# Kernel tuning notes

Hardware: AMD Instinct MI355X
Metric: run time of the kernel (lower is better)

Reference implementation:

```python
import jax, jax.numpy as jnp
import numpy as np

# TT embedding config
IN_SHAPE = (100, 100, 100)      # vocab = 1_000_000
OUT_SHAPE = (4, 8, 4)           # embed_dim = 128
RANKS = (1, 32, 32, 32, 16, 8, 1)
OUT_SIZE = int(np.prod(OUT_SHAPE))
VOCAB = int(np.prod(IN_SHAPE))

def _xavier(key, shape):
    fan_in, fan_out = shape[0] * shape[1], shape[1] * shape[2]
    a = float(np.sqrt(6.0 / (shape[0] * shape[1] * shape[2] / shape[1] + 0)))  # placeholder
    # torch xavier_uniform on (r0, n, r1): fan_in = n*r1? torch treats dim0 as fan_out-ish;
    # exact init scale does not affect correctness checking, use a simple uniform bound.
    bound = float(np.sqrt(6.0 / (shape[0] * shape[1] + shape[1] * shape[2])))
    return jax.random.uniform(key, shape, jnp.float32, -bound, bound)

def setup_inputs() -> dict:
    key = jax.random.key(0)
    ks = jax.random.split(key, 7)
    idx = jax.random.randint(ks[0], (512, 128), 0, VOCAB, dtype=jnp.int32)
    shapes = [(RANKS[i], s, RANKS[i + 1]) for i, s in enumerate(IN_SHAPE + OUT_SHAPE)]
    cores = [_xavier(ks[i + 1], shapes[i]) for i in range(6)]
    return {"idx": idx, "core0": cores[0], "core1": cores[1], "core2": cores[2],
            "core3": cores[3], "core4": cores[4], "core5": cores[5]}

def reference(idx, core0, core1, core2, core3, core4, core5):
    in_shape = idx.shape
    flat = idx.reshape(-1)  # [N]
    # index decomposition with tt_index_factor = [10000, 100]
    i0 = flat // 10000
    i1 = (flat % 10000) // 100
    i2 = flat % 100
    # per-index gather + chained small batched matmuls over input cores
    g = core0[0, i0, :]                              # [N, r1]
    g = jnp.einsum('nr,rns->ns', g, core1[:, i1, :])  # [N, r2]
    g = jnp.einsum('nr,rns->ns', g, core2[:, i2, :])  # [N, r3]
    # contract output cores into a single [r3, OUT_SIZE] matrix (shared across batch)
    t = core3.reshape(-1, core4.shape[0]) @ core4.reshape(core4.shape[0], -1)
    t = t.reshape(-1, core5.shape[0]) @ core5.reshape(core5.shape[0], -1)
    W = t.reshape(RANKS[3], OUT_SIZE)                # [r3, 128]
    out = g @ W                                      # [N, 128]
    return out.reshape(in_shape + (OUT_SIZE,))
```

## Files before the change

kernel.cpp:

```cpp
#include <hip/hip_runtime.h>

#define N_TOKENS   65536
#define TOKS_PER_BLK 128
#define MAIN_TILES (N_TOKENS / TOKS_PER_BLK + 100)
#define ORD_SIZE    (MAIN_TILES * TOKS_PER_BLK)
#define NB_M2   400
#define NB_G1T  1250
#define NB_HIST 64
#define PREP_BLOCKS (NB_M2 + NB_G1T + NB_HIST)

#define WS_M2T  0
#define WS_G1T  204800
#define WS_CNT  364800
#define WS_ORD  372992
#define WS_NEED ((size_t)(372992 + ORD_SIZE) * 4)

typedef __attribute__((ext_vector_type(8))) short bf16x8;
typedef __attribute__((ext_vector_type(4))) float f32x4;

__device__ __forceinline__ unsigned short f2bf(float x) {
    union { float f; unsigned u; } v; v.f = x;
    unsigned r = v.u + 0x7FFF + ((v.u >> 16) & 1);
    return (unsigned short)(r >> 16);
}

__global__ __launch_bounds__(256) void prep(
    const int* __restrict__ idx,
    const float* __restrict__ c0, const float* __restrict__ c1,
    const float* __restrict__ c2, const float* __restrict__ c3,
    const float* __restrict__ c4, const float* __restrict__ c5,
    unsigned short* __restrict__ M2T, unsigned short* __restrict__ G1Tb,
    int* __restrict__ cntT) {
    __shared__ float smem[5200];
    const int b = blockIdx.x, t = threadIdx.x;

    if (b < NB_M2) {
        const int i2 = b >> 2;
        const int p  = b & 3;
        float* c4l = smem;
        float* c5l = smem + 1024;
        float* t45 = smem + 1056;
        float* c3p = smem + 1568;
        float* Wl  = smem + 2080;
        float* c2l = smem + 3104;
        *(float4*)(c4l + t * 4) = *(const float4*)(c4 + t * 4);
        if (t < 8) *(float4*)(c5l + t * 4) = *(const float4*)(c5 + t * 4);
        if (t < 128) {
            const int r = t >> 2, q4 = (t & 3) * 4;
            *(float4*)(c3p + r * 16 + q4) = *(const float4*)(c3 + (r * 4 + p) * 16 + q4);
        }
        {
            const int r = t >> 3, s4 = (t & 7) * 4;
            const float4 v = *(const float4*)(c2 + r * 3200 + i2 * 32 + s4);
            c2l[r * 33 + s4 + 0] = v.x;
            c2l[r * 33 + s4 + 1] = v.y;
            c2l[r * 33 + s4 + 2] = v.z;
            c2l[r * 33 + s4 + 3] = v.w;
        }
        __syncthreads();
#pragma unroll
        for (int k = 0; k < 2; ++k) {
            const int e = t + k * 256;
            const int q = e >> 5, u = e & 31;
            const int m1 = u >> 2, v = u & 3;
            float acc = 0.f;
#pragma unroll
            for (int m2 = 0; m2 < 8; ++m2)
                acc = fmaf(c4l[q * 64 + m1 * 8 + m2], c5l[m2 * 4 + v], acc);
            t45[e] = acc;
        }
        __syncthreads();
#pragma unroll
        for (int k = 0; k < 4; ++k) {
            const int e = t + k * 256;
            const int s = e >> 5, jl = e & 31;
            float acc = 0.f;
#pragma unroll
            for (int q = 0; q < 16; ++q)
                acc = fmaf(c3p[s * 16 + q], t45[q * 32 + jl], acc);
            Wl[e] = acc;
        }
        __syncthreads();
#pragma unroll
        for (int k = 0; k < 4; ++k) {
            const int e = t + k * 256;
            const int jl = e >> 5, r = e & 31;
            float acc = 0.f;
#pragma unroll
            for (int s = 0; s < 32; ++s)
                acc = fmaf(c2l[r * 33 + s], Wl[s * 32 + jl], acc);
            M2T[i2 * 4096 + p * 1024 + e] = f2bf(acc);
        }
    } else if (b < NB_M2 + NB_G1T) {
        const int pair = (b - NB_M2) * 8 + (t >> 5);
        const int s = t & 31;
        const int i0 = pair / 100;
        const int i1 = pair - i0 * 100;
        const float4* a4 = (const float4*)(c0 + i0 * 32);
        const float* c1p = c1 + i1 * 32 + s;
        float acc = 0.f;
#pragma unroll
        for (int r4 = 0; r4 < 8; ++r4) {
            const float4 a = a4[r4];
            acc = fmaf(a.x, c1p[(r4 * 4 + 0) * 3200], acc);
            acc = fmaf(a.y, c1p[(r4 * 4 + 1) * 3200], acc);
            acc = fmaf(a.z, c1p[(r4 * 4 + 2) * 3200], acc);
            acc = fmaf(a.w, c1p[(r4 * 4 + 3) * 3200], acc);
        }
        G1Tb[pair * 32 + s] = f2bf(acc);
    } else {
        const int hb = b - (NB_M2 + NB_G1T);
        int* lh = (int*)smem;
        if (t < 128) lh[t] = 0;
        __syncthreads();
#pragma unroll
        for (int k = 0; k < 4; ++k) {
            const int n = hb * 1024 + k * 256 + t;
            atomicAdd(&lh[idx[n] % 100], 1);
        }
        __syncthreads();
        if (t < 128) cntT[t * 64 + hb] = lh[t];
    }
}

__global__ __launch_bounds__(256) void sort2(const int* __restrict__ idx,
                                             const int* __restrict__ cntT,
                                             int* __restrict__ order) {
    __shared__ int totals[100];
    __shared__ int offsj[100];
    __shared__ int sb[101];
    __shared__ int lhj[100];
    const int j = blockIdx.x, t = threadIdx.x;
    if (t < 100) {
        lhj[t] = 0;
        const int4* row = (const int4*)(cntT + t * 64);
        int tot = 0, off = 0;
#pragma unroll
        for (int i = 0; i < 16; ++i) {
            const int4 v = row[i];
            const int cb = i * 4;
            tot += v.x + v.y + v.z + v.w;
            if (cb + 0 < j) off += v.x;
            if (cb + 1 < j) off += v.y;
            if (cb + 2 < j) off += v.z;
            if (cb + 3 < j) off += v.w;
        }
        totals[t] = tot;
        offsj[t] = off;
    }
    __syncthreads();
    if (t < 64) {
        const int e0 = 2 * t, e1 = 2 * t + 1;
        const int p0 = (e0 < 100) ? ((totals[e0] + 127) & ~127) : 0;
        const int p1 = (e1 < 100) ? ((totals[e1] + 127) & ~127) : 0;
        const int pair = p0 + p1;
        int incl = pair;
#pragma unroll
        for (int d = 1; d < 64; d <<= 1) {
            const int v = __shfl_up(incl, d, 64);
            if (t >= d) incl += v;
        }
        const int base = incl - pair;
        if (e0 < 100) sb[e0] = base;
        if (e1 < 100) sb[e1] = base + p0;
        if (t == 63) sb[100] = incl;
    }
    __syncthreads();
    int bkt[4], rnk[4];
#pragma unroll
    for (int k = 0; k < 4; ++k) {
        const int n = j * 1024 + k * 256 + t;
        const int bb = idx[n] % 100;
        bkt[k] = bb;
        rnk[k] = atomicAdd(&lhj[bb], 1);
    }
#pragma unroll
    for (int k = 0; k < 4; ++k) {
        const int n = j * 1024 + k * 256 + t;
        order[sb[bkt[k]] + offsj[bkt[k]] + rnk[k]] = n;
    }
    for (int bb = j; bb < 100; bb += 64) {
        const int tot = totals[bb];
        const int pt = (tot + 127) & ~127;
        for (int i = tot + t; i < pt; i += 256) order[sb[bb] + i] = -1;
    }
    {
        const int gt = sb[100];
        for (int i = gt + j * 256 + t; i < ORD_SIZE; i += 64 * 256) order[i] = -1;
    }
}

__global__ __launch_bounds__(256) void tt_main(
    const int* __restrict__ idx, const int* __restrict__ order,
    const unsigned short* __restrict__ G1Tb, const unsigned short* __restrict__ M2T,
    float* __restrict__ out) {
    __shared__ unsigned short g1b[128 * 40];
    __shared__ unsigned short m2t[128 * 40];
    __shared__ int toks[TOKS_PER_BLK];

    const int t = threadIdx.x;
    const int base = blockIdx.x * TOKS_PER_BLK;
    const int n0 = order[base];
    if (n0 < 0) return;
    const int i2v = idx[n0] % 100;

    {
        const int tk = t >> 1, half = t & 1;
        const int n = order[base + tk];
        int4 v0 = {0, 0, 0, 0}, v1 = {0, 0, 0, 0};
        if (n >= 0) {
            const int pair = idx[n] / 100;
            const int4* g = (const int4*)(G1Tb + pair * 32);
            v0 = g[half * 2];
            v1 = g[half * 2 + 1];
        }
        int4* d = (int4*)(g1b + tk * 40 + half * 16);
        d[0] = v0;
        d[1] = v1;
        if (t < TOKS_PER_BLK) toks[t] = order[base + t];
    }
    {
        const int j = t >> 1, half = t & 1;
        const int4* s = (const int4*)(M2T + i2v * 4096 + j * 32);
        int4* d = (int4*)(m2t + j * 40 + half * 16);
        d[0] = s[half * 2];
        d[1] = s[half * 2 + 1];
    }
    __syncthreads();

    const int wid  = t >> 6;
    const int lane = t & 63;
    const int ln15 = lane & 15;
    const int q8   = (lane >> 4) * 8;

    f32x4 acc[2][8];
#pragma unroll
    for (int a = 0; a < 2; ++a)
#pragma unroll
        for (int c = 0; c < 8; ++c) acc[a][c] = (f32x4){0.f, 0.f, 0.f, 0.f};

    bf16x8 af[2], bfr[8];
#pragma unroll
    for (int trr = 0; trr < 2; ++trr) {
        const int tok = (2 * wid + trr) * 16 + ln15;
        af[trr] = *(const bf16x8*)(g1b + tok * 40 + q8);
    }
#pragma unroll
    for (int tc = 0; tc < 8; ++tc) {
        const int j = tc * 16 + ln15;
        bfr[tc] = *(const bf16x8*)(m2t + j * 40 + q8);
    }
#pragma unroll
    for (int trr = 0; trr < 2; ++trr)
#pragma unroll
        for (int tc = 0; tc < 8; ++tc)
            acc[trr][tc] = __builtin_amdgcn_mfma_f32_16x16x32_bf16(
                af[trr], bfr[tc], acc[trr][tc], 0, 0, 0);

    const int rowq = (lane >> 4) * 4;
#pragma unroll
    for (int trr = 0; trr < 2; ++trr) {
#pragma unroll
        for (int reg = 0; reg < 4; ++reg) {
            const int tokr = (2 * wid + trr) * 16 + rowq + reg;
            const int n = toks[tokr];
            if (n >= 0) {
                float* o = out + (size_t)n * 128 + ln15;
#pragma unroll
                for (int tc = 0; tc < 8; ++tc) o[tc * 16] = acc[trr][tc][reg];
            }
        }
    }
}

__global__ void build_w(const float* __restrict__ c3, const float* __restrict__ c4,
                        const float* __restrict__ c5, float* __restrict__ W) {
    int t = blockIdx.x * blockDim.x + threadIdx.x;
    if (t >= 32 * 128) return;
    int r = t >> 7;
    int j = t & 127;
    int p  = j >> 5;
    int m1 = (j >> 2) & 7;
    int v  = j & 3;
    const float* c3row = c3 + (r * 4 + p) * 16;
    float acc = 0.f;
#pragma unroll
    for (int m2 = 0; m2 < 8; ++m2) {
        float t1 = 0.f;
#pragma unroll
        for (int q = 0; q < 16; ++q)
            t1 += c3row[q] * c4[q * 64 + m1 * 8 + m2];
        acc += t1 * c5[m2 * 4 + v];
    }
    W[r * 128 + j] = acc;
}

__global__ __launch_bounds__(256, 4) void tt_embed_fb(
    const int* __restrict__ idx, const float* __restrict__ c0,
    const float* __restrict__ c1, const float* __restrict__ c2,
    const float* __restrict__ Wg, float* __restrict__ out) {
    __shared__ float Wl[32 * 128];
    __shared__ float g2l[8][32];
    const int t = threadIdx.x;
    {
        const float4* Wg4 = (const float4*)Wg;
        float4* Wl4 = (float4*)Wl;
#pragma unroll
        for (int i = 0; i < 4; ++i) Wl4[t + i * 256] = Wg4[t + i * 256];
    }
    __syncthreads();
    const int tt = t >> 5, s = t & 31;
    const int blockBase = blockIdx.x * 32;
    for (int round = 0; round < 4; ++round) {
        const int n = blockBase + round * 8 + tt;
        const int iv = idx[n];
        const int i0 = iv / 10000;
        const int rem = iv - i0 * 10000;
        const int i1 = rem / 100;
        const int i2 = rem - i1 * 100;
        const float4* c0r4 = (const float4*)(c0 + i0 * 32);
        const float* c1p = c1 + i1 * 32 + s;
        float g1 = 0.f;
#pragma unroll
        for (int r4 = 0; r4 < 8; ++r4) {
            float4 a = c0r4[r4];
            g1 += a.x * c1p[(r4 * 4 + 0) * 3200];
            g1 += a.y * c1p[(r4 * 4 + 1) * 3200];
            g1 += a.z * c1p[(r4 * 4 + 2) * 3200];
            g1 += a.w * c1p[(r4 * 4 + 3) * 3200];
        }
        const float* c2p = c2 + i2 * 32 + s;
        float g2 = 0.f;
#pragma unroll
        for (int r = 0; r < 32; ++r) {
            float g1r = __shfl(g1, r, 32);
            g2 += g1r * c2p[r * 3200];
        }
        g2l[tt][s] = g2;
        __syncthreads();
        float4 acc = {0.f, 0.f, 0.f, 0.f};
        const float4* Wl4 = (const float4*)Wl;
#pragma unroll
        for (int r = 0; r < 32; ++r) {
            const float g = g2l[tt][r];
            const float4 w = Wl4[r * 32 + s];
            acc.x += g * w.x; acc.y += g * w.y; acc.z += g * w.z; acc.w += g * w.w;
        }
        float4* outp = (float4*)(out + (size_t)n * 128);
        outp[s] = acc;
        __syncthreads();
    }
}

extern "C" void kernel_launch(void* const* d_in, const int* in_sizes, int n_in,
                              void* d_out, int out_size, void* d_ws, size_t ws_size,
                              hipStream_t stream) {
    const int*   idx = (const int*)d_in[0];
    const float* c0  = (const float*)d_in[1];
    const float* c1  = (const float*)d_in[2];
    const float* c2  = (const float*)d_in[3];
    const float* c3  = (const float*)d_in[4];
    const float* c4  = (const float*)d_in[5];
    const float* c5  = (const float*)d_in[6];
    float* out = (float*)d_out;
    float* ws  = (float*)d_ws;

    if (ws_size >= WS_NEED) {
        unsigned short* M2T  = (unsigned short*)(ws + WS_M2T);
        unsigned short* G1Tb = (unsigned short*)(ws + WS_G1T);
        int* cntT  = (int*)(ws + WS_CNT);
        int* order = (int*)(ws + WS_ORD);

        hipLaunchKernelGGL(prep,  dim3(PREP_BLOCKS), dim3(256), 0, stream,
                           idx, c0, c1, c2, c3, c4, c5, M2T, G1Tb, cntT);
        hipLaunchKernelGGL(sort2, dim3(NB_HIST), dim3(256), 0, stream, idx, cntT, order);
        hipLaunchKernelGGL(tt_main, dim3(MAIN_TILES), dim3(256), 0, stream,
                           idx, order, G1Tb, M2T, out);
    } else {
        float* W = ws;
        hipLaunchKernelGGL(build_w, dim3(16), dim3(256), 0, stream, c3, c4, c5, W);
        hipLaunchKernelGGL(tt_embed_fb, dim3(N_TOKENS / 32), dim3(256), 0, stream,
                           idx, c0, c1, c2, W, out);
    }
}
```

Baseline: 26.80 us.

## Split main tiles across two output halves and widen the sort grid

The histogram/sort stage now uses 256 chunks of 256 tokens instead of 64 chunks of 1024, so each sort block handles one token per thread and the grid is four times larger. The main MFMA kernel launches two blocks per token tile, each computing 64 of the 128 output columns, which halves per-block LDS and accumulator registers and doubles the block count. The intent is more parallelism and occupancy on a GPU with many CUs. The cost is that the G1 row gather and token order are loaded twice per tile, and the sort kernel scans longer count rows (256 entries per bucket per block).

```diff
diff --git a/kernel.cpp b/kernel.cpp
--- a/kernel.cpp
+++ b/kernel.cpp
@@ -3,17 +3,19 @@
 #define N_TOKENS   65536
 #define TOKS_PER_BLK 128
 #define MAIN_TILES (N_TOKENS / TOKS_PER_BLK + 100)
+#define MAIN_BLOCKS (MAIN_TILES * 2)
 #define ORD_SIZE    (MAIN_TILES * TOKS_PER_BLK)
 #define NB_M2   400
 #define NB_G1T  1250
-#define NB_HIST 64
+#define NB_HIST 256
+#define NCHUNK  256
 #define PREP_BLOCKS (NB_M2 + NB_G1T + NB_HIST)
 
 #define WS_M2T  0
 #define WS_G1T  204800
 #define WS_CNT  364800
-#define WS_ORD  372992
-#define WS_NEED ((size_t)(372992 + ORD_SIZE) * 4)
+#define WS_ORD  397568
+#define WS_NEED ((size_t)(397568 + ORD_SIZE) * 4)
 
 typedef __attribute__((ext_vector_type(8))) short bf16x8;
 typedef __attribute__((ext_vector_type(4))) float f32x4;
@@ -113,13 +115,9 @@
         int* lh = (int*)smem;
         if (t < 128) lh[t] = 0;
         __syncthreads();
-#pragma unroll
-        for (int k = 0; k < 4; ++k) {
-            const int n = hb * 1024 + k * 256 + t;
-            atomicAdd(&lh[idx[n] % 100], 1);
-        }
-        __syncthreads();
-        if (t < 128) cntT[t * 64 + hb] = lh[t];
+        atomicAdd(&lh[idx[hb * 256 + t] % 100], 1);
+        __syncthreads();
+        if (t < 128) cntT[t * NCHUNK + hb] = lh[t];
     }
 }
 
@@ -133,10 +131,10 @@
     const int j = blockIdx.x, t = threadIdx.x;
     if (t < 100) {
         lhj[t] = 0;
-        const int4* row = (const int4*)(cntT + t * 64);
+        const int4* row = (const int4*)(cntT + t * NCHUNK);
         int tot = 0, off = 0;
 #pragma unroll
-        for (int i = 0; i < 16; ++i) {
+        for (int i = 0; i < NCHUNK / 4; ++i) {
             const int4 v = row[i];
             const int cb = i * 4;
             tot += v.x + v.y + v.z + v.w;
@@ -166,27 +164,20 @@
         if (t == 63) sb[100] = incl;
     }
     __syncthreads();
-    int bkt[4], rnk[4];
-#pragma unroll
-    for (int k = 0; k < 4; ++k) {
-        const int n = j * 1024 + k * 256 + t;
+    {
+        const int n = j * 256 + t;
         const int bb = idx[n] % 100;
-        bkt[k] = bb;
-        rnk[k] = atomicAdd(&lhj[bb], 1);
-    }
-#pragma unroll
-    for (int k = 0; k < 4; ++k) {
-        const int n = j * 1024 + k * 256 + t;
-        order[sb[bkt[k]] + offsj[bkt[k]] + rnk[k]] = n;
-    }
-    for (int bb = j; bb < 100; bb += 64) {
-        const int tot = totals[bb];
+        const int rnk = atomicAdd(&lhj[bb], 1);
+        order[sb[bb] + offsj[bb] + rnk] = n;
+    }
+    if (j < 100) {
+        const int tot = totals[j];
         const int pt = (tot + 127) & ~127;
-        for (int i = tot + t; i < pt; i += 256) order[sb[bb] + i] = -1;
+        for (int i = tot + t; i < pt; i += 256) order[sb[j] + i] = -1;
     }
     {
         const int gt = sb[100];
-        for (int i = gt + j * 256 + t; i < ORD_SIZE; i += 64 * 256) order[i] = -1;
+        for (int i = gt + j * 256 + t; i < ORD_SIZE; i += NCHUNK * 256) order[i] = -1;
     }
 }
 
@@ -195,11 +186,13 @@
     const unsigned short* __restrict__ G1Tb, const unsigned short* __restrict__ M2T,
     float* __restrict__ out) {
     __shared__ unsigned short g1b[128 * 40];
-    __shared__ unsigned short m2t[128 * 40];
+    __shared__ unsigned short m2t[64 * 40];
     __shared__ int toks[TOKS_PER_BLK];
 
     const int t = threadIdx.x;
-    const int base = blockIdx.x * TOKS_PER_BLK;
+    const int tile = blockIdx.x >> 1;
+    const int ch   = blockIdx.x & 1;
+    const int base = tile * TOKS_PER_BLK;
     const int n0 = order[base];
     if (n0 < 0) return;
     const int i2v = idx[n0] % 100;
@@ -220,11 +213,9 @@
         if (t < TOKS_PER_BLK) toks[t] = order[base + t];
     }
     {
-        const int j = t >> 1, half = t & 1;
-        const int4* s = (const int4*)(M2T + i2v * 4096 + j * 32);
-        int4* d = (int4*)(m2t + j * 40 + half * 16);
-        d[0] = s[half * 2];
-        d[1] = s[half * 2 + 1];
+        const int j = t >> 2, q = t & 3;
+        const int4* s = (const int4*)(M2T + i2v * 4096 + (ch * 64 + j) * 32);
+        ((int4*)(m2t + j * 40))[q] = s[q];
     }
     __syncthreads();
 
@@ -233,27 +224,27 @@
     const int ln15 = lane & 15;
     const int q8   = (lane >> 4) * 8;
 
-    f32x4 acc[2][8];
+    f32x4 acc[2][4];
 #pragma unroll
     for (int a = 0; a < 2; ++a)
 #pragma unroll
-        for (int c = 0; c < 8; ++c) acc[a][c] = (f32x4){0.f, 0.f, 0.f, 0.f};
-
-    bf16x8 af[2], bfr[8];
+        for (int c = 0; c < 4; ++c) acc[a][c] = (f32x4){0.f, 0.f, 0.f, 0.f};
+
+    bf16x8 af[2], bfr[4];
 #pragma unroll
     for (int trr = 0; trr < 2; ++trr) {
         const int tok = (2 * wid + trr) * 16 + ln15;
         af[trr] = *(const bf16x8*)(g1b + tok * 40 + q8);
     }
 #pragma unroll
-    for (int tc = 0; tc < 8; ++tc) {
+    for (int tc = 0; tc < 4; ++tc) {
         const int j = tc * 16 + ln15;
         bfr[tc] = *(const bf16x8*)(m2t + j * 40 + q8);
     }
 #pragma unroll
     for (int trr = 0; trr < 2; ++trr)
 #pragma unroll
-        for (int tc = 0; tc < 8; ++tc)
+        for (int tc = 0; tc < 4; ++tc)
             acc[trr][tc] = __builtin_amdgcn_mfma_f32_16x16x32_bf16(
                 af[trr], bfr[tc], acc[trr][tc], 0, 0, 0);
 
@@ -265,9 +256,9 @@
             const int tokr = (2 * wid + trr) * 16 + rowq + reg;
             const int n = toks[tokr];
             if (n >= 0) {
-                float* o = out + (size_t)n * 128 + ln15;
-#pragma unroll
-                for (int tc = 0; tc < 8; ++tc) o[tc * 16] = acc[trr][tc][reg];
+                float* o = out + (size_t)n * 128 + ch * 64 + ln15;
+#pragma unroll
+                for (int tc = 0; tc < 4; ++tc) o[tc * 16] = acc[trr][tc][reg];
             }
         }
     }
@@ -373,8 +364,8 @@
 
         hipLaunchKernelGGL(prep,  dim3(PREP_BLOCKS), dim3(256), 0, stream,
                            idx, c0, c1, c2, c3, c4, c5, M2T, G1Tb, cntT);
-        hipLaunchKernelGGL(sort2, dim3(NB_HIST), dim3(256), 0, stream, idx, cntT, order);
-        hipLaunchKernelGGL(tt_main, dim3(MAIN_TILES), dim3(256), 0, stream,
+        hipLaunchKernelGGL(sort2, dim3(NCHUNK), dim3(256), 0, stream, idx, cntT, order);
+        hipLaunchKernelGGL(tt_main, dim3(MAIN_BLOCKS), dim3(256), 0, stream,
                            idx, order, G1Tb, M2T, out);
     } else {
         float* W = ws;
```

New measurement: 28.99 us. +8.2%, slower.
